# Kernel tuning notes

Hardware: AMD Instinct MI355X
Metric: run time of the kernel (lower is better)

Reference implementation:

```python
import jax, jax.numpy as jnp
import numpy as np


def setup_inputs() -> dict:
    key = jax.random.key(0)
    ks = jax.random.split(key, 8)
    N, T, U = 8, 512, 64
    E, D, J, V = 512, 512, 512, 500
    s = 0.02
    return {
        "encoder_out": jax.random.normal(ks[0], (N, T, E), jnp.float32),
        "decoder_out": jax.random.normal(ks[1], (N, U, D), jnp.float32),
        "W_enc": jax.random.normal(ks[2], (J, E), jnp.float32) * s,
        "b_enc": jnp.zeros((J,), jnp.float32),
        "W_dec": jax.random.normal(ks[3], (J, D), jnp.float32) * s,
        "b_dec": jnp.zeros((J,), jnp.float32),
        "W_out": jax.random.normal(ks[4], (V, J), jnp.float32) * s,
        "b_out": jnp.zeros((V,), jnp.float32),
    }


def reference(encoder_out, decoder_out, W_enc, b_enc, W_dec, b_dec, W_out, b_out):
    # Project encoder [N,T,E]->[N,T,J] and decoder [N,U,D]->[N,U,J]
    enc = jnp.einsum("nte,je->ntj", encoder_out, W_enc) + b_enc
    dec = jnp.einsum("nud,jd->nuj", decoder_out, W_dec) + b_dec
    # Broadcast add over (T,U), tanh, then vocab projection -> [N,T,U,V]
    activations = jnp.tanh(enc[:, :, None, :] + dec[:, None, :, :])
    logits = jnp.einsum("ntuj,vj->ntuv", activations, W_out) + b_out
    return logits
```

## Files before the change

kernel.cpp:

```cpp
#include <hip/hip_runtime.h>
#include <hip/hip_bf16.h>


typedef __attribute__((ext_vector_type(4))) float f32x4;
typedef __attribute__((ext_vector_type(16))) float f32x16;
typedef __attribute__((ext_vector_type(4))) short s16x4;
typedef __attribute__((ext_vector_type(8))) short s16x8;

static __device__ __forceinline__ unsigned short f2bf(float x) {
    union { float f; unsigned u; } v; v.f = x;
    return (unsigned short)((v.u + 0x7FFFu + ((v.u >> 16) & 1u)) >> 16);
}

static __device__ __forceinline__ float fast_tanh(float x) {
    float e = __expf(2.0f * x);
    float r = __builtin_amdgcn_rcpf(e + 1.0f);
    return __builtin_fmaf(-2.0f, r, 1.0f);
}

static __device__ __forceinline__ unsigned swz64(int r, int c) {
    return (unsigned)(r * 64 + ((c ^ ((r >> 1) & 3)) << 4));
}

static __device__ void proj_body(
    const float* __restrict__ A, const float* __restrict__ W,
    const float* __restrict__ b, float* __restrict__ C,
    int mt, int jt, unsigned short* As, unsigned short* Bs)
{
    const int tid = threadIdx.x;
    const int lane = tid & 63, wid = tid >> 6;
    const int wm = wid >> 1, wn = wid & 1;

    f32x4 acc[4][4];
    const f32x4 zero = {0.f, 0.f, 0.f, 0.f};
    #pragma unroll
    for (int i = 0; i < 4; ++i)
        #pragma unroll
        for (int j = 0; j < 4; ++j) acc[i][j] = zero;

    const int c8 = (tid & 7) * 8;
    const int rbase = tid >> 3;

    for (int kt = 0; kt < 8; ++kt) {
        __syncthreads();
        #pragma unroll
        for (int p = 0; p < 4; ++p) {
            int r = p * 32 + rbase;
            int byte = (r * 128 + c8 * 2) ^ ((r & 7) << 4);
            {
                const float* s = A + (size_t)(mt * 128 + r) * 512 + kt * 64 + c8;
                f32x4 v0 = *(const f32x4*)s, v1 = *(const f32x4*)(s + 4);
                s16x8 pk;
                pk[0] = (short)f2bf(v0[0]); pk[1] = (short)f2bf(v0[1]);
                pk[2] = (short)f2bf(v0[2]); pk[3] = (short)f2bf(v0[3]);
                pk[4] = (short)f2bf(v1[0]); pk[5] = (short)f2bf(v1[1]);
                pk[6] = (short)f2bf(v1[2]); pk[7] = (short)f2bf(v1[3]);
                *(s16x8*)((char*)As + byte) = pk;
            }
            {
                const float* s = W + (size_t)(jt * 128 + r) * 512 + kt * 64 + c8;
                f32x4 v0 = *(const f32x4*)s, v1 = *(const f32x4*)(s + 4);
                s16x8 pk;
                pk[0] = (short)f2bf(v0[0]); pk[1] = (short)f2bf(v0[1]);
                pk[2] = (short)f2bf(v0[2]); pk[3] = (short)f2bf(v0[3]);
                pk[4] = (short)f2bf(v1[0]); pk[5] = (short)f2bf(v1[1]);
                pk[6] = (short)f2bf(v1[2]); pk[7] = (short)f2bf(v1[3]);
                *(s16x8*)((char*)Bs + byte) = pk;
            }
        }
        __syncthreads();
        #pragma unroll
        for (int kk = 0; kk < 2; ++kk) {
            s16x8 af[4], bfr[4];
            #pragma unroll
            for (int mi = 0; mi < 4; ++mi) {
                int row = wm * 64 + mi * 16 + (lane & 15);
                int byte = (row * 128 + kk * 64 + ((lane >> 4) * 16)) ^ ((row & 7) << 4);
                af[mi] = *(const s16x8*)((const char*)As + byte);
            }
            #pragma unroll
            for (int ni = 0; ni < 4; ++ni) {
                int row = wn * 64 + ni * 16 + (lane & 15);
                int byte = (row * 128 + kk * 64 + ((lane >> 4) * 16)) ^ ((row & 7) << 4);
                bfr[ni] = *(const s16x8*)((const char*)Bs + byte);
            }
            #pragma unroll
            for (int mi = 0; mi < 4; ++mi)
                #pragma unroll
                for (int ni = 0; ni < 4; ++ni)
                    acc[mi][ni] = __builtin_amdgcn_mfma_f32_16x16x32_bf16(
                        af[mi], bfr[ni], acc[mi][ni], 0, 0, 0);
        }
    }

    #pragma unroll
    for (int ni = 0; ni < 4; ++ni) {
        int col = jt * 128 + wn * 64 + ni * 16 + (lane & 15);
        float bias = b[col];
        #pragma unroll
        for (int mi = 0; mi < 4; ++mi) {
            int row0 = mt * 128 + wm * 64 + mi * 16 + ((lane >> 4) << 2);
            #pragma unroll
            for (int j = 0; j < 4; ++j)
                C[(size_t)(row0 + j) * 512 + col] = acc[mi][ni][j] + bias;
        }
    }
}

__global__ __launch_bounds__(256) void prep(
    const float* __restrict__ Wout, unsigned short* __restrict__ img,
    const float* __restrict__ encoder_out, const float* __restrict__ W_enc,
    const float* __restrict__ b_enc, float* __restrict__ enc_p,
    const float* __restrict__ decoder_out, const float* __restrict__ W_dec,
    const float* __restrict__ b_dec, float* __restrict__ dec_p)
{
    __shared__ unsigned short As[128 * 64];
    __shared__ unsigned short Bs[128 * 64];
    const int b = blockIdx.x;
    if (b < 128) {
        int tid = b * 256 + threadIdx.x;
        int lane = tid & 63;
        int khalf = (tid >> 6) & 1;
        int tile = (tid >> 7) & 15;
        int kt = tid >> 11;
        int v = tile * 32 + (lane & 31);
        int k = kt * 32 + khalf * 16 + (lane >> 5) * 8;
        s16x8 pk = {0, 0, 0, 0, 0, 0, 0, 0};
        if (v < 500) {
            const float* s = Wout + (size_t)v * 512 + k;
            f32x4 a = *(const f32x4*)s, c = *(const f32x4*)(s + 4);
            pk[0] = (short)f2bf(a[0]); pk[1] = (short)f2bf(a[1]);
            pk[2] = (short)f2bf(a[2]); pk[3] = (short)f2bf(a[3]);
            pk[4] = (short)f2bf(c[0]); pk[5] = (short)f2bf(c[1]);
            pk[6] = (short)f2bf(c[2]); pk[7] = (short)f2bf(c[3]);
        }
        *(s16x8*)(img + (size_t)tid * 8) = pk;
    } else if (b < 256) {
        int q = b - 128;
        proj_body(encoder_out, W_enc, b_enc, enc_p, q & 31, q >> 5, As, Bs);
    } else {
        int q = b - 256;
        proj_body(decoder_out, W_dec, b_dec, dec_p, q & 3, q >> 2, As, Bs);
    }
}

__global__ __launch_bounds__(512, 4) void joiner_main(
    const float* __restrict__ enc, const float* __restrict__ dec,
    const unsigned short* __restrict__ Wimg, const float* __restrict__ bout,
    float* __restrict__ out)
{
    __shared__ __align__(16) char raw[8192 + 33024];
    unsigned short* As0 = (unsigned short*)raw;
    unsigned short* As1 = (unsigned short*)(raw + 4096);
    float* ep = (float*)(raw + 8192);

    const int bid = blockIdx.x;
    const int tid = threadIdx.x, lane = tid & 63, wn = tid >> 6;
    const int n = bid >> 9, t = bid & 511;

    f32x16 acc[2][2];
    #pragma unroll
    for (int i = 0; i < 2; ++i)
        #pragma unroll
        for (int j = 0; j < 2; ++j)
            #pragma unroll
            for (int e = 0; e < 16; ++e) acc[i][j][e] = 0.f;

    const int r = tid >> 3;
    const int q8 = tid & 7;
    const float* erow = enc + ((size_t)n * 512 + t) * 512 + q8 * 4;
    const float* drow = dec + ((size_t)n * 64 + r) * 512 + q8 * 4;
    const unsigned abyte = swz64(r, q8 >> 1) + (q8 & 1) * 8;
    const char* wbase = (const char*)Wimg + (size_t)wn * 4096 + (size_t)lane * 16;
    const int lr = lane & 31, kg = lane >> 5;

    {
        f32x4 e0 = *(const f32x4*)erow;
        f32x4 d0 = *(const f32x4*)drow;
        s16x4 p;
        p[0] = (short)f2bf(fast_tanh(e0[0] + d0[0]));
        p[1] = (short)f2bf(fast_tanh(e0[1] + d0[1]));
        p[2] = (short)f2bf(fast_tanh(e0[2] + d0[2]));
        p[3] = (short)f2bf(fast_tanh(e0[3] + d0[3]));
        *(s16x4*)((char*)As0 + abyte) = p;
    }
    __syncthreads();

    #pragma unroll
    for (int kt = 0; kt < 16; ++kt) {
        const char* Ac = (char*)((kt & 1) ? As1 : As0);
        char* An = (char*)((kt & 1) ? As0 : As1);

        s16x8 bfr[2][2];
        {
            const char* g = wbase + (size_t)kt * 32768;
            #pragma unroll
            for (int ni = 0; ni < 2; ++ni)
                #pragma unroll
                for (int kh = 0; kh < 2; ++kh)
                    bfr[ni][kh] = *(const s16x8*)(g + ni * 2048 + kh * 1024);
        }
        s16x8 af[2][2];
        #pragma unroll
        for (int mi = 0; mi < 2; ++mi)
            #pragma unroll
            for (int kh = 0; kh < 2; ++kh)
                af[mi][kh] = *(const s16x8*)(Ac + swz64(mi * 32 + lr, kh * 2 + kg));
        if (kt < 15) {
            const float* e_ = erow + (kt + 1) * 32;
            const float* d_ = drow + (kt + 1) * 32;
            f32x4 e0 = *(const f32x4*)e_;
            f32x4 d0 = *(const f32x4*)d_;
            s16x4 p;
            p[0] = (short)f2bf(fast_tanh(e0[0] + d0[0]));
            p[1] = (short)f2bf(fast_tanh(e0[1] + d0[1]));
            p[2] = (short)f2bf(fast_tanh(e0[2] + d0[2]));
            p[3] = (short)f2bf(fast_tanh(e0[3] + d0[3]));
            *(s16x4*)(An + abyte) = p;
        }
        #pragma unroll
        for (int kh = 0; kh < 2; ++kh)
            #pragma unroll
            for (int mi = 0; mi < 2; ++mi)
                #pragma unroll
                for (int ni = 0; ni < 2; ++ni)
                    acc[mi][ni] = __builtin_amdgcn_mfma_f32_32x32x16_bf16(
                        bfr[ni][kh], af[mi][kh], acc[mi][ni], 0, 0, 0);
        __syncthreads();
    }

    const int hi4 = (lane >> 5) * 4;
    const int lr16 = lane & 15;
    #pragma unroll
    for (int o = 0; o < 4; ++o) {
        __syncthreads();
        if (((lane >> 4) & 1) == (o & 1)) {
            const int mi = o >> 1;
            #pragma unroll
            for (int ni = 0; ni < 2; ++ni) {
                #pragma unroll
                for (int q = 0; q < 4; ++q) {
                    int v4 = wn * 64 + ni * 32 + q * 8 + hi4;
                    f32x4 b = *(const f32x4*)(bout + v4);
                    f32x4 ov;
                    ov[0] = acc[mi][ni == 0 ? 0 : 1][q * 4 + 0] + b[0];
                    ov[1] = acc[mi][ni == 0 ? 0 : 1][q * 4 + 1] + b[1];
                    ov[2] = acc[mi][ni == 0 ? 0 : 1][q * 4 + 2] + b[2];
                    ov[3] = acc[mi][ni == 0 ? 0 : 1][q * 4 + 3] + b[3];
                    *(f32x4*)(ep + lr16 * 516 + v4) = ov;
                }
            }
        }
        __syncthreads();
        const size_t obase = ((size_t)bid * 64 + o * 16) * 500;
        #pragma unroll
        for (int i = 0; i < 4; ++i) {
            int idx = i * 512 + tid;
            if (idx < 2000) {
                int rr = idx / 125;
                int vi = (idx - rr * 125) * 4;
                f32x4 ov = *(const f32x4*)(ep + rr * 516 + vi);
                __builtin_nontemporal_store(ov, (f32x4*)(out + obase + (size_t)idx * 4));
            }
        }
    }
}

extern "C" void kernel_launch(void* const* d_in, const int* in_sizes, int n_in,
                              void* d_out, int out_size, void* d_ws, size_t ws_size,
                              hipStream_t stream) {
    const float* encoder_out = (const float*)d_in[0];
    const float* decoder_out = (const float*)d_in[1];
    const float* W_enc = (const float*)d_in[2];
    const float* b_enc = (const float*)d_in[3];
    const float* W_dec = (const float*)d_in[4];
    const float* b_dec = (const float*)d_in[5];
    const float* W_out = (const float*)d_in[6];
    const float* b_out = (const float*)d_in[7];
    float* out = (float*)d_out;

    float* enc_p = (float*)d_ws;
    float* dec_p = enc_p + (size_t)8 * 512 * 512;
    unsigned short* wimg = (unsigned short*)(dec_p + (size_t)8 * 64 * 512);
    float* bpad = (float*)(wimg + (size_t)8 * 65536 / 2 * 2);

    prep<<<dim3(272), 256, 0, stream>>>(W_out, wimg,
                                        encoder_out, W_enc, b_enc, enc_p,
                                        decoder_out, W_dec, b_dec, dec_p);
    hipMemsetAsync(bpad, 0, 512 * sizeof(float), stream);
    hipMemcpyAsync(bpad, b_out, 500 * sizeof(float), hipMemcpyDeviceToDevice, stream);
    joiner_main<<<dim3(4096), 512, 0, stream>>>(enc_p, dec_p, wimg, bpad, out);
}
```

Baseline: 239.1 us.

## Store projections in bf16, fold bias padding into prep, widen epilogue staging

The encoder and decoder projections are now written as bf16 instead of fp32, which halves the reads of enc/dec in the main joiner loop. The memset and memcpy that padded b_out become an extra block in the prep kernel, removing two stream operations. The joiner now reuses the whole LDS region for output staging and stores 32 rows per pass in two passes instead of four, which cuts barriers. It also interleaves B-fragment loads with the MFMAs. Raising LDS to 66 KB per block may lower occupancy, and rounding the projections to bf16 adds precision loss before the tanh.

```diff
diff --git a/kernel.cpp b/kernel.cpp
--- a/kernel.cpp
+++ b/kernel.cpp
@@ -6,10 +6,16 @@
 typedef __attribute__((ext_vector_type(16))) float f32x16;
 typedef __attribute__((ext_vector_type(4))) short s16x4;
 typedef __attribute__((ext_vector_type(8))) short s16x8;
+typedef __attribute__((ext_vector_type(4))) unsigned short u16x4;
 
 static __device__ __forceinline__ unsigned short f2bf(float x) {
     union { float f; unsigned u; } v; v.f = x;
     return (unsigned short)((v.u + 0x7FFFu + ((v.u >> 16) & 1u)) >> 16);
+}
+
+static __device__ __forceinline__ float bf2f(unsigned short u) {
+    union { unsigned u; float f; } v; v.u = ((unsigned)u) << 16;
+    return v.f;
 }
 
 static __device__ __forceinline__ float fast_tanh(float x) {
@@ -24,7 +30,7 @@
 
 static __device__ void proj_body(
     const float* __restrict__ A, const float* __restrict__ W,
-    const float* __restrict__ b, float* __restrict__ C,
+    const float* __restrict__ b, unsigned short* __restrict__ C,
     int mt, int jt, unsigned short* As, unsigned short* Bs)
 {
     const int tid = threadIdx.x;
@@ -102,7 +108,7 @@
             int row0 = mt * 128 + wm * 64 + mi * 16 + ((lane >> 4) << 2);
             #pragma unroll
             for (int j = 0; j < 4; ++j)
-                C[(size_t)(row0 + j) * 512 + col] = acc[mi][ni][j] + bias;
+                C[(size_t)(row0 + j) * 512 + col] = f2bf(acc[mi][ni][j] + bias);
         }
     }
 }
@@ -110,9 +116,10 @@
 __global__ __launch_bounds__(256) void prep(
     const float* __restrict__ Wout, unsigned short* __restrict__ img,
     const float* __restrict__ encoder_out, const float* __restrict__ W_enc,
-    const float* __restrict__ b_enc, float* __restrict__ enc_p,
+    const float* __restrict__ b_enc, unsigned short* __restrict__ enc_p,
     const float* __restrict__ decoder_out, const float* __restrict__ W_dec,
-    const float* __restrict__ b_dec, float* __restrict__ dec_p)
+    const float* __restrict__ b_dec, unsigned short* __restrict__ dec_p,
+    const float* __restrict__ b_out, float* __restrict__ bpad)
 {
     __shared__ unsigned short As[128 * 64];
     __shared__ unsigned short Bs[128 * 64];
@@ -138,21 +145,25 @@
     } else if (b < 256) {
         int q = b - 128;
         proj_body(encoder_out, W_enc, b_enc, enc_p, q & 31, q >> 5, As, Bs);
-    } else {
+    } else if (b < 272) {
         int q = b - 256;
         proj_body(decoder_out, W_dec, b_dec, dec_p, q & 3, q >> 2, As, Bs);
+    } else {
+        int i = threadIdx.x;
+        bpad[i] = (i < 500) ? b_out[i] : 0.f;
+        bpad[i + 256] = (i + 256 < 500) ? b_out[i + 256] : 0.f;
     }
 }
 
 __global__ __launch_bounds__(512, 4) void joiner_main(
-    const float* __restrict__ enc, const float* __restrict__ dec,
+    const unsigned short* __restrict__ enc, const unsigned short* __restrict__ dec,
     const unsigned short* __restrict__ Wimg, const float* __restrict__ bout,
     float* __restrict__ out)
 {
-    __shared__ __align__(16) char raw[8192 + 33024];
+    __shared__ __align__(16) char raw[66048];
     unsigned short* As0 = (unsigned short*)raw;
     unsigned short* As1 = (unsigned short*)(raw + 4096);
-    float* ep = (float*)(raw + 8192);
+    float* ep = (float*)raw;
 
     const int bid = blockIdx.x;
     const int tid = threadIdx.x, lane = tid & 63, wn = tid >> 6;
@@ -167,21 +178,21 @@
             for (int e = 0; e < 16; ++e) acc[i][j][e] = 0.f;
 
     const int r = tid >> 3;
-    const int q8 = tid & 7;
-    const float* erow = enc + ((size_t)n * 512 + t) * 512 + q8 * 4;
-    const float* drow = dec + ((size_t)n * 64 + r) * 512 + q8 * 4;
-    const unsigned abyte = swz64(r, q8 >> 1) + (q8 & 1) * 8;
+    const int q = tid & 7;
+    const unsigned short* erow = enc + ((size_t)n * 512 + t) * 512 + q * 4;
+    const unsigned short* drow = dec + ((size_t)n * 64 + r) * 512 + q * 4;
+    const unsigned abyte = swz64(r, q >> 1) + (q & 1) * 8;
     const char* wbase = (const char*)Wimg + (size_t)wn * 4096 + (size_t)lane * 16;
     const int lr = lane & 31, kg = lane >> 5;
 
     {
-        f32x4 e0 = *(const f32x4*)erow;
-        f32x4 d0 = *(const f32x4*)drow;
+        u16x4 e = *(const u16x4*)erow;
+        u16x4 d = *(const u16x4*)drow;
         s16x4 p;
-        p[0] = (short)f2bf(fast_tanh(e0[0] + d0[0]));
-        p[1] = (short)f2bf(fast_tanh(e0[1] + d0[1]));
-        p[2] = (short)f2bf(fast_tanh(e0[2] + d0[2]));
-        p[3] = (short)f2bf(fast_tanh(e0[3] + d0[3]));
+        p[0] = (short)f2bf(fast_tanh(bf2f(e[0]) + bf2f(d[0])));
+        p[1] = (short)f2bf(fast_tanh(bf2f(e[1]) + bf2f(d[1])));
+        p[2] = (short)f2bf(fast_tanh(bf2f(e[2]) + bf2f(d[2])));
+        p[3] = (short)f2bf(fast_tanh(bf2f(e[3]) + bf2f(d[3])));
         *(s16x4*)((char*)As0 + abyte) = p;
     }
     __syncthreads();
@@ -190,73 +201,61 @@
     for (int kt = 0; kt < 16; ++kt) {
         const char* Ac = (char*)((kt & 1) ? As1 : As0);
         char* An = (char*)((kt & 1) ? As0 : As1);
-
-        s16x8 bfr[2][2];
+        const char* g = wbase + (size_t)kt * 32768;
+
+        if (kt < 15) {
+            u16x4 e = *(const u16x4*)(erow + (kt + 1) * 32);
+            u16x4 d = *(const u16x4*)(drow + (kt + 1) * 32);
+            s16x4 p;
+            p[0] = (short)f2bf(fast_tanh(bf2f(e[0]) + bf2f(d[0])));
+            p[1] = (short)f2bf(fast_tanh(bf2f(e[1]) + bf2f(d[1])));
+            p[2] = (short)f2bf(fast_tanh(bf2f(e[2]) + bf2f(d[2])));
+            p[3] = (short)f2bf(fast_tanh(bf2f(e[3]) + bf2f(d[3])));
+            *(s16x4*)(An + abyte) = p;
+        }
+        #pragma unroll
+        for (int kh = 0; kh < 2; ++kh) {
+            s16x8 b0 = *(const s16x8*)(g + 0 * 2048 + kh * 1024);
+            s16x8 b1 = *(const s16x8*)(g + 1 * 2048 + kh * 1024);
+            s16x8 a0 = *(const s16x8*)(Ac + swz64(lr, kh * 2 + kg));
+            s16x8 a1 = *(const s16x8*)(Ac + swz64(32 + lr, kh * 2 + kg));
+            acc[0][0] = __builtin_amdgcn_mfma_f32_32x32x16_bf16(b0, a0, acc[0][0], 0, 0, 0);
+            acc[0][1] = __builtin_amdgcn_mfma_f32_32x32x16_bf16(b1, a0, acc[0][1], 0, 0, 0);
+            acc[1][0] = __builtin_amdgcn_mfma_f32_32x32x16_bf16(b0, a1, acc[1][0], 0, 0, 0);
+            acc[1][1] = __builtin_amdgcn_mfma_f32_32x32x16_bf16(b1, a1, acc[1][1], 0, 0, 0);
+        }
+        __syncthreads();
+    }
+
+    const int hi4 = (lane >> 5) * 4;
+    #pragma unroll
+    for (int o = 0; o < 2; ++o) {
+        if (o) __syncthreads();
         {
-            const char* g = wbase + (size_t)kt * 32768;
-            #pragma unroll
-            for (int ni = 0; ni < 2; ++ni)
-                #pragma unroll
-                for (int kh = 0; kh < 2; ++kh)
-                    bfr[ni][kh] = *(const s16x8*)(g + ni * 2048 + kh * 1024);
-        }
-        s16x8 af[2][2];
-        #pragma unroll
-        for (int mi = 0; mi < 2; ++mi)
-            #pragma unroll
-            for (int kh = 0; kh < 2; ++kh)
-                af[mi][kh] = *(const s16x8*)(Ac + swz64(mi * 32 + lr, kh * 2 + kg));
-        if (kt < 15) {
-            const float* e_ = erow + (kt + 1) * 32;
-            const float* d_ = drow + (kt + 1) * 32;
-            f32x4 e0 = *(const f32x4*)e_;
-            f32x4 d0 = *(const f32x4*)d_;
-            s16x4 p;
-            p[0] = (short)f2bf(fast_tanh(e0[0] + d0[0]));
-            p[1] = (short)f2bf(fast_tanh(e0[1] + d0[1]));
-            p[2] = (short)f2bf(fast_tanh(e0[2] + d0[2]));
-            p[3] = (short)f2bf(fast_tanh(e0[3] + d0[3]));
-            *(s16x4*)(An + abyte) = p;
-        }
-        #pragma unroll
-        for (int kh = 0; kh < 2; ++kh)
-            #pragma unroll
-            for (int mi = 0; mi < 2; ++mi)
-                #pragma unroll
-                for (int ni = 0; ni < 2; ++ni)
-                    acc[mi][ni] = __builtin_amdgcn_mfma_f32_32x32x16_bf16(
-                        bfr[ni][kh], af[mi][kh], acc[mi][ni], 0, 0, 0);
-        __syncthreads();
-    }
-
-    const int hi4 = (lane >> 5) * 4;
-    const int lr16 = lane & 15;
-    #pragma unroll
-    for (int o = 0; o < 4; ++o) {
-        __syncthreads();
-        if (((lane >> 4) & 1) == (o & 1)) {
-            const int mi = o >> 1;
+            const int mi = o;
             #pragma unroll
             for (int ni = 0; ni < 2; ++ni) {
                 #pragma unroll
-                for (int q = 0; q < 4; ++q) {
-                    int v4 = wn * 64 + ni * 32 + q * 8 + hi4;
-                    f32x4 b = *(const f32x4*)(bout + v4);
-                    f32x4 ov;
-                    ov[0] = acc[mi][ni == 0 ? 0 : 1][q * 4 + 0] + b[0];
-                    ov[1] = acc[mi][ni == 0 ? 0 : 1][q * 4 + 1] + b[1];
-                    ov[2] = acc[mi][ni == 0 ? 0 : 1][q * 4 + 2] + b[2];
-                    ov[3] = acc[mi][ni == 0 ? 0 : 1][q * 4 + 3] + b[3];
-                    *(f32x4*)(ep + lr16 * 516 + v4) = ov;
+                for (int qq = 0; qq < 4; ++qq) {
+                    int v4 = wn * 64 + ni * 32 + qq * 8 + hi4;
+                    if (v4 < 500) {
+                        f32x4 b = *(const f32x4*)(bout + v4);
+                        f32x4 ov;
+                        ov[0] = acc[mi][ni][qq * 4 + 0] + b[0];
+                        ov[1] = acc[mi][ni][qq * 4 + 1] + b[1];
+                        ov[2] = acc[mi][ni][qq * 4 + 2] + b[2];
+                        ov[3] = acc[mi][ni][qq * 4 + 3] + b[3];
+                        *(f32x4*)(ep + lr * 516 + v4) = ov;
+                    }
                 }
             }
         }
         __syncthreads();
-        const size_t obase = ((size_t)bid * 64 + o * 16) * 500;
-        #pragma unroll
-        for (int i = 0; i < 4; ++i) {
+        const size_t obase = ((size_t)bid * 64 + o * 32) * 500;
+        #pragma unroll
+        for (int i = 0; i < 8; ++i) {
             int idx = i * 512 + tid;
-            if (idx < 2000) {
+            if (idx < 4000) {
                 int rr = idx / 125;
                 int vi = (idx - rr * 125) * 4;
                 f32x4 ov = *(const f32x4*)(ep + rr * 516 + vi);
@@ -279,15 +278,14 @@
     const float* b_out = (const float*)d_in[7];
     float* out = (float*)d_out;
 
-    float* enc_p = (float*)d_ws;
-    float* dec_p = enc_p + (size_t)8 * 512 * 512;
-    unsigned short* wimg = (unsigned short*)(dec_p + (size_t)8 * 64 * 512);
-    float* bpad = (float*)(wimg + (size_t)8 * 65536 / 2 * 2);
-
-    prep<<<dim3(272), 256, 0, stream>>>(W_out, wimg,
+    unsigned short* enc_p = (unsigned short*)d_ws;
+    unsigned short* dec_p = enc_p + (size_t)4096 * 512;
+    unsigned short* wimg  = dec_p + (size_t)512 * 512;
+    float* bpad = (float*)(wimg + 262144);
+
+    prep<<<dim3(273), 256, 0, stream>>>(W_out, wimg,
                                         encoder_out, W_enc, b_enc, enc_p,
-                                        decoder_out, W_dec, b_dec, dec_p);
-    hipMemsetAsync(bpad, 0, 512 * sizeof(float), stream);
-    hipMemcpyAsync(bpad, b_out, 500 * sizeof(float), hipMemcpyDeviceToDevice, stream);
+                                        decoder_out, W_dec, b_dec, dec_p,
+                                        b_out, bpad);
     joiner_main<<<dim3(4096), 512, 0, stream>>>(enc_p, dec_p, wimg, bpad, out);
 }
```

Measured after the change: 225.6 us. 5.6% less time.
